# Optimization experiments

Measured on AMD Instinct MI355X. Metric: run time of the kernel, lower is better.

## Reference

```python
import jax, jax.numpy as jnp
from jax import lax
import numpy as np

Z, Y, X = 41, 256, 256  # sparse_shape = grid_size[::-1]
N_VOX = 60000
C_IN = 4
DN = ('NCDHW', 'OIDHW', 'NCDHW')


def _conv(x, w, stride=(1, 1, 1), pad=1):
    return lax.conv_general_dilated(x, w, stride, [(pad, pad)] * 3, dimension_numbers=DN)


def _tconv(x, w, stride=(2, 2, 2), pad=1, outpad=(0, 0, 0)):
    # torch ConvTranspose3d (weight [Cin,Cout,k,k,k]) == conv with lhs dilation,
    # spatially-flipped, in/out-swapped kernel, padding (k-1-p, k-1-p+output_padding)
    wt = jnp.flip(jnp.swapaxes(w, 0, 1), axis=(2, 3, 4))
    padding = [(2 - pad, 2 - pad + op) for op in outpad]  # k=3
    return lax.conv_general_dilated(x, wt, (1, 1, 1), padding, lhs_dilation=stride, dimension_numbers=DN)


def _bn_relu(y, s, b, m):
    # eval-mode BN folded into per-channel scale/shift, then ReLU, then restrict
    # to the sparse active-site mask (spconv only stores features at active sites)
    return jax.nn.relu(y * s[None, :, None, None, None] + b[None, :, None, None, None]) * m


def _forward(feats, params, coords, batch_size):
    (w1, s1, b1, w2a, s2a, b2a, w2b, s2b, b2b, w3a, s3a, b3a, w3b, s3b, b3b,
     w4a, s4a, b4a, w4b, s4b, b4b, w5a, s5a, b5a, w5b, s5b, b5b) = params
    B = batch_size
    bi, zi, yi, xi = coords[:, 0], coords[:, 1], coords[:, 2], coords[:, 3]
    dense = jnp.zeros((B, C_IN, Z, Y, X), feats.dtype).at[bi, :, zi, yi, xi].set(feats)
    m0 = jnp.zeros((B, 1, Z, Y, X), feats.dtype).at[bi, 0, zi, yi, xi].set(1.0)
    one = jnp.ones((1, 1, 3, 3, 3), feats.dtype)
    # conv1: SparseConv3d k3 s1 p1 -> active set dilates
    m1 = (_conv(m0, one) > 0).astype(feats.dtype)
    x = _bn_relu(_conv(dense, w1), s1, b1, m1)
    # conv2: SparseConv3d s2 + SubMConv3d (mask unchanged for subm)
    m2 = (_conv(m1, one, (2, 2, 2)) > 0).astype(feats.dtype)
    x = _bn_relu(_conv(x, w2a, (2, 2, 2)), s2a, b2a, m2)
    x = _bn_relu(_conv(x, w2b), s2b, b2b, m2)
    # conv3
    m3 = (_conv(m2, one, (2, 2, 2)) > 0).astype(feats.dtype)
    x = _bn_relu(_conv(x, w3a, (2, 2, 2)), s3a, b3a, m3)
    x = _bn_relu(_conv(x, w3b), s3b, b3b, m3)
    # deconv4: SparseConvTranspose3d s2 + subm
    m4 = (_tconv(m3, one) > 0).astype(feats.dtype)
    x = _bn_relu(_tconv(x, w4a), s4a, b4a, m4)
    x = _bn_relu(_conv(x, w4b), s4b, b4b, m4)
    # deconv5: output_padding (0,3,3) restores full Y/X resolution
    m5 = (_tconv(m4, one, outpad=(0, 3, 3)) > 0).astype(feats.dtype)
    x = _bn_relu(_tconv(x, w5a, outpad=(0, 3, 3)), s5a, b5a, m5)
    x = _bn_relu(_conv(x, w5b), s5b, b5b, m5)
    return x  # dense [B, 32, Z, Y, X]; zeros at inactive sites


def setup_inputs() -> dict:
    rng = np.random.default_rng(0)
    flat = rng.choice(Z * Y * X, size=N_VOX, replace=False)
    zi = (flat // (Y * X)).astype(np.int32)
    rem = flat % (Y * X)
    yi = (rem // X).astype(np.int32)
    xi = (rem % X).astype(np.int32)
    coords = np.stack([np.zeros(N_VOX, np.int32), zi, yi, xi], axis=1)

    def w(o, i):
        return jnp.asarray((rng.standard_normal((o, i, 3, 3, 3)) * 0.05).astype(np.float32))

    def scale(c):
        return jnp.asarray(rng.uniform(0.5, 1.5, c).astype(np.float32))

    def shift(c):
        return jnp.asarray((rng.standard_normal(c) * 0.1).astype(np.float32))

    return {
        'occ_voxel_features': jnp.asarray(rng.standard_normal((N_VOX, C_IN)).astype(np.float32)),
        'occ_voxel_coords': jnp.asarray(coords),
        'batch_size': 1,
        'w1': w(16, 4), 's1': scale(16), 'b1': shift(16),
        'w2a': w(32, 16), 's2a': scale(32), 'b2a': shift(32),
        'w2b': w(32, 32), 's2b': scale(32), 'b2b': shift(32),
        'w3a': w(64, 32), 's3a': scale(64), 'b3a': shift(64),
        'w3b': w(64, 64), 's3b': scale(64), 'b3b': shift(64),
        'w4a': w(64, 32), 's4a': scale(32), 'b4a': shift(32),  # transpose weight [Cin,Cout,...]
        'w4b': w(32, 32), 's4b': scale(32), 'b4b': shift(32),
        'w5a': w(32, 32), 's5a': scale(32), 'b5a': shift(32),
        'w5b': w(32, 32), 's5b': scale(32), 'b5b': shift(32),
    }


def reference(occ_voxel_features, occ_voxel_coords, batch_size,
              w1, s1, b1, w2a, s2a, b2a, w2b, s2b, b2b,
              w3a, s3a, b3a, w3b, s3b, b3b,
              w4a, s4a, b4a, w4b, s4b, b4b,
              w5a, s5a, b5a, w5b, s5b, b5b):
    params = (w1, s1, b1, w2a, s2a, b2a, w2b, s2b, b2b, w3a, s3a, b3a, w3b, s3b, b3b,
              w4a, s4a, b4a, w4b, s4b, b4b, w5a, s5a, b5a, w5b, s5b, b5b)
    return _forward(occ_voxel_features, params, occ_voxel_coords, batch_size)
```

## Files before the change

kernel.cpp:

```cpp
#include <hip/hip_runtime.h>
#include <hip/hip_bf16.h>
#include <stdint.h>

namespace {

constexpr int Z0 = 41, Y0 = 256, X0 = 256;
constexpr int Z2 = 21, Y2 = 128, X2 = 128;
constexpr int Z3 = 11, Y3 = 64,  X3 = 64;
constexpr int Z4 = 21, Y4 = 127, X4 = 127;
constexpr int NV0 = Z0 * Y0 * X0;
constexpr int NV2 = Z2 * Y2 * X2;
constexpr int NV3 = Z3 * Y3 * X3;
constexpr int NV4 = Z4 * Y4 * X4;

constexpr int ZP0 = 43, YP0 = 258, XP0 = 258; constexpr int NP0 = ZP0 * YP0 * XP0;
constexpr int ZP2 = 23, YP2 = 130, XP2 = 130; constexpr int NP2 = ZP2 * YP2 * XP2;
constexpr int ZP3 = 13, YP3 = 66,  XP3 = 66;  constexpr int NP3 = ZP3 * YP3 * XP3;
constexpr int ZP4 = 23, YP4 = 129, XP4 = 129; constexpr int NP4 = ZP4 * YP4 * XP4;

using bf16 = __hip_bfloat16;
typedef __attribute__((ext_vector_type(8))) short s16x8;
typedef __attribute__((ext_vector_type(4))) float f32x4;

__device__ inline unsigned f2b(float f) {
    return (unsigned)__builtin_bit_cast(unsigned short, __float2bfloat16(f));
}

__device__ inline int xcd_swz(int bid, int nwg) {
    int q = nwg >> 3, r = nwg & 7;
    int x = bid & 7, j = bid >> 3;
    return (x < r ? x * (q + 1) : r * (q + 1) + (x - r) * q) + j;
}

__device__ inline void glds16(const bf16* g, void* l) {
    __builtin_amdgcn_global_load_lds(
        (const __attribute__((address_space(1))) void*)g,
        (__attribute__((address_space(3))) void*)l, 16, 0, 0);
}

__global__ __launch_bounds__(256) void sentinel_k(float* out) { out[0] = 12345.0f; }

__global__ __launch_bounds__(256) void scatter_k(const float* __restrict__ feats,
                                                 const int* __restrict__ coords,
                                                 bf16* __restrict__ dense,
                                                 uint8_t* __restrict__ m0, int n) {
    int v = blockIdx.x * 256 + threadIdx.x;
    if (v >= n) return;
    int z = coords[v * 4 + 1], y = coords[v * 4 + 2], x = coords[v * 4 + 3];
    m0[(z * Y0 + y) * X0 + x] = 1;
    int pp = ((z + 1) * YP0 + (y + 1)) * XP0 + (x + 1);
    uint2 u;
    u.x = f2b(feats[v * 4 + 0]) | (f2b(feats[v * 4 + 1]) << 16);
    u.y = f2b(feats[v * 4 + 2]) | (f2b(feats[v * 4 + 3]) << 16);
    *(uint2*)(dense + (size_t)pp * 4) = u;
}

template <int C>
__global__ __launch_bounds__(256) void halo_zero_k(bf16* __restrict__ buf,
                                                   int Zi, int Yi, int Xi,
                                                   int Zp, int Yp, int Xp) {
    int i = blockIdx.x * 256 + threadIdx.x;
    int tot = Zp * Yp * Xp;
    if (i >= tot) return;
    int x = i % Xp; int t = i / Xp; int y = t % Yp; int z = t / Yp;
    bool halo = (z < 1) | (z > Zi) | (y < 1) | (y > Yi) | (x < 1) | (x > Xi);
    if (!halo) return;
    uint4 zz = make_uint4(0, 0, 0, 0);
    uint4* p = (uint4*)(buf + (size_t)i * C);
#pragma unroll
    for (int j = 0; j < C / 8; ++j) p[j] = zz;
}

__global__ __launch_bounds__(256) void repack_frag_k(const float* __restrict__ w,
                                                     bf16* __restrict__ wf,
                                                     int CIN, int COUT, int TRANS) {
    int NT = COUT / 16, KT = CIN / 32;
    int i = blockIdx.x * 256 + threadIdx.x;
    int total = 27 * NT * KT * 64;
    if (i >= total) return;
    int lane = i & 63; int t = i >> 6;
    int kt = t % KT; t /= KT; int nt = t % NT; int tap = t / NT;
    int co = nt * 16 + (lane & 15);
    int ci0 = kt * 32 + (lane >> 4) * 8;
    unsigned e[8];
#pragma unroll
    for (int j = 0; j < 8; ++j) {
        int ci = ci0 + j;
        int src = TRANS ? ((ci * COUT + co) * 27 + tap) : ((co * CIN + ci) * 27 + tap);
        e[j] = f2b(w[src]);
    }
    uint4 u;
    u.x = e[0] | (e[1] << 16); u.y = e[2] | (e[3] << 16);
    u.z = e[4] | (e[5] << 16); u.w = e[6] | (e[7] << 16);
    ((uint4*)wf)[i] = u;
}

__global__ __launch_bounds__(256) void repack_frag_c16_k(const float* __restrict__ w,
                                                         bf16* __restrict__ wf) {
    int i = blockIdx.x * 256 + threadIdx.x;
    int total = 14 * 2 * 64;
    if (i >= total) return;
    int lane = i & 63; int t = i >> 6;
    int nt = t & 1; int p = t >> 1;
    int lg = lane >> 4, lr = lane & 15;
    int co = nt * 16 + lr;
    unsigned e[8];
#pragma unroll
    for (int j = 0; j < 8; ++j) {
        int tap = 2 * p + (lg >> 1);
        int ci = (lg & 1) * 8 + j;
        e[j] = (tap < 27) ? f2b(w[(co * 16 + ci) * 27 + tap]) : 0u;
    }
    uint4 u;
    u.x = e[0] | (e[1] << 16); u.y = e[2] | (e[3] << 16);
    u.z = e[4] | (e[5] << 16); u.w = e[6] | (e[7] << 16);
    ((uint4*)wf)[i] = u;
}

__global__ __launch_bounds__(256) void repack_frag_l1_k(const float* __restrict__ w,
                                                        bf16* __restrict__ wf) {
    int i = blockIdx.x * 256 + threadIdx.x;
    if (i >= 256) return;
    int lane = i & 63, kb = i >> 6;
    int lg = lane >> 4, lr = lane & 15;
    unsigned e[8];
#pragma unroll
    for (int j = 0; j < 8; ++j) {
        int tap = kb * 8 + lg * 2 + (j >> 2);
        int ci = j & 3;
        e[j] = (tap < 27) ? f2b(w[(lr * 4 + ci) * 27 + tap]) : 0u;
    }
    uint4 u;
    u.x = e[0] | (e[1] << 16); u.y = e[2] | (e[3] << 16);
    u.z = e[4] | (e[5] << 16); u.w = e[6] | (e[7] << 16);
    ((uint4*)wf)[i] = u;
}

__global__ __launch_bounds__(256) void dilate_k(const uint8_t* __restrict__ in,
                                                uint8_t* __restrict__ out,
                                                int Zi, int Yi, int Xi,
                                                int Zo, int Yo, int Xo, int stride) {
    int idx = blockIdx.x * 256 + threadIdx.x;
    int total = Zo * Yo * Xo;
    if (idx >= total) return;
    int x = idx % Xo; int t = idx / Xo; int y = t % Yo; int z = t / Yo;
    int YX = Yi * Xi;
    uint8_t r = 0;
    for (int kz = 0; kz < 3; ++kz) {
        int zi = z * stride + kz - 1;
        if ((unsigned)zi >= (unsigned)Zi) continue;
        for (int ky = 0; ky < 3; ++ky) {
            int yi = y * stride + ky - 1;
            if ((unsigned)yi >= (unsigned)Yi) continue;
            for (int kx = 0; kx < 3; ++kx) {
                int xi = x * stride + kx - 1;
                if ((unsigned)xi >= (unsigned)Xi) continue;
                r |= in[zi * YX + yi * Xi + xi];
            }
        }
    }
    out[idx] = r ? 1 : 0;
}

__global__ __launch_bounds__(256) void dilate4_k(const uint8_t* __restrict__ in,
                                                 uint8_t* __restrict__ out,
                                                 int Z, int Y, int X) {
    int ngx = X >> 2;
    int g = blockIdx.x * 256 + threadIdx.x;
    int total = Z * Y * ngx;
    if (g >= total) return;
    int gx = g % ngx; int t = g / ngx; int y = t % Y; int z = t / Y;
    const int YX = Y * X;
    unsigned r = 0;
    for (int kz = 0; kz < 3; ++kz) {
        int zi = z + kz - 1;
        if ((unsigned)zi >= (unsigned)Z) continue;
        for (int ky = 0; ky < 3; ++ky) {
            int yi = y + ky - 1;
            if ((unsigned)yi >= (unsigned)Y) continue;
            const unsigned* rw = (const unsigned*)(in + zi * YX + yi * X);
            unsigned u1 = rw[gx];
            unsigned u0 = gx ? rw[gx - 1] : 0u;
            unsigned u2 = (gx + 1 < ngx) ? rw[gx + 1] : 0u;
            r |= u1 | ((u1 << 8) | (u0 >> 24)) | ((u1 >> 8) | (u2 << 24));
        }
    }
    r |= r >> 4; r |= r >> 2; r |= r >> 1; r &= 0x01010101u;
    ((unsigned*)out)[g] = r;
}

__global__ __launch_bounds__(256) void tdilate_k(const uint8_t* __restrict__ in,
                                                 uint8_t* __restrict__ out,
                                                 int Zi, int Yi, int Xi,
                                                 int Zo, int Yo, int Xo) {
    int idx = blockIdx.x * 256 + threadIdx.x;
    int total = Zo * Yo * Xo;
    if (idx >= total) return;
    int x = idx % Xo; int t = idx / Xo; int y = t % Yo; int z = t / Yo;
    int YX = Yi * Xi;
    uint8_t r = 0;
    for (int kz = 0; kz < 3; ++kz) {
        int tz = z + 1 - kz;
        if (tz & 1) continue;
        int zi = tz >> 1;
        if ((unsigned)zi >= (unsigned)Zi) continue;
        for (int ky = 0; ky < 3; ++ky) {
            int ty = y + 1 - ky;
            if (ty & 1) continue;
            int yi = ty >> 1;
            if ((unsigned)yi >= (unsigned)Yi) continue;
            for (int kx = 0; kx < 3; ++kx) {
                int tx = x + 1 - kx;
                if (tx & 1) continue;
                int xi = tx >> 1;
                if ((unsigned)xi >= (unsigned)Xi) continue;
                r |= in[zi * YX + yi * Xi + xi];
            }
        }
    }
    out[idx] = r ? 1 : 0;
}

__global__ __launch_bounds__(256) void tdilate4_k(const uint8_t* __restrict__ in,
                                                  uint8_t* __restrict__ out,
                                                  int Zi, int Yi, int Xi,
                                                  int Zo, int Yo, int Xo) {
    int ngx = Xo >> 2;
    int g = blockIdx.x * 256 + threadIdx.x;
    int total = Zo * Yo * ngx;
    if (g >= total) return;
    int gx = g % ngx; int t = g / ngx; int y = t % Yo; int z = t / Yo;
    int YX = Yi * Xi;
    int j0 = gx * 2;
    unsigned r0 = 0, r1 = 0, r2 = 0, r3 = 0;
    for (int kz = 0; kz < 3; ++kz) {
        int tz = z + 1 - kz;
        if (tz & 1) continue;
        int zi = tz >> 1;
        if ((unsigned)zi >= (unsigned)Zi) continue;
        for (int ky = 0; ky < 3; ++ky) {
            int ty = y + 1 - ky;
            if (ty & 1) continue;
            int yi = ty >> 1;
            if ((unsigned)yi >= (unsigned)Yi) continue;
            const uint8_t* rp = in + zi * YX + yi * Xi;
            unsigned b0 = (j0 < Xi) ? rp[j0] : 0u;
            unsigned b1 = (j0 + 1 < Xi) ? rp[j0 + 1] : 0u;
            unsigned b2 = (j0 + 2 < Xi) ? rp[j0 + 2] : 0u;
            r0 |= b0; r1 |= b0 | b1; r2 |= b1; r3 |= b1 | b2;
        }
    }
    unsigned rr = (r0 ? 1u : 0u) | (r1 ? 0x100u : 0u) | (r2 ? 0x10000u : 0u) | (r3 ? 0x1000000u : 0u);
    ((unsigned*)out)[g] = rr;
}

__global__ __launch_bounds__(256, 3) void conv_roll_k(
    const bf16* __restrict__ in, const bf16* __restrict__ wfrag,
    const float* __restrict__ scale, const float* __restrict__ shift,
    const uint8_t* __restrict__ mask, float* __restrict__ outf,
    int Zo, int Yo, int Xo, int Ypi, int Xpi, int nx) {
    constexpr int ROWB = 34 * 64;
    constexpr int SLABB = 4 * ROWB;
    __shared__ uint4 ring4[4 * SLABB / 16];
    char* ring = (char*)ring4;

    const int No = Zo * Yo * Xo;
    const int bid = xcd_swz(blockIdx.x, gridDim.x);
    const int tx = bid % nx, ty = bid / nx;
    const int y0 = ty * 2, x0 = tx * 32;

    const int tid = threadIdx.x;
    const int w = tid >> 6, lane = tid & 63;
    const int lg = lane >> 4, lr = lane & 15;
    const int yr = w >> 1, ch = w & 1;

    auto stage = [&](int zp) {
        int zs = zp <= Zo + 1 ? zp : Zo + 1;
        char* slab = ring + (zp & 3) * SLABB + w * ROWB;
        const bf16* pb = in + ((size_t)zs * Ypi + (y0 + w)) * (size_t)Xpi * 32 + (size_t)x0 * 32;
#pragma unroll
        for (int k = 0; k < 3; ++k) {
            int u = k * 64 + lane;
            if (k < 2 || lane < 8) {
                int usw = u ^ ((u >> 3) & 7);
                glds16(pb + usw * 8, slab + u * 16);
            }
        }
    };

    const uint4* gw = (const uint4*)wfrag;
    uint4 breg[27];
#pragma unroll
    for (int t = 0; t < 27; ++t) breg[t] = gw[(t * 2 + ch) * 64 + lane];

    stage(0); stage(1); stage(2);

    int asw[2][3];
#pragma unroll
    for (int xh = 0; xh < 2; ++xh)
#pragma unroll
        for (int dx = 0; dx < 3; ++dx) {
            int b = (xh * 16 + lr + dx) * 64 + lg * 16;
            asw[xh][dx] = b ^ (((b >> 7) & 7) << 4);
        }

    const int co = ch * 16 + lr;
    const float sc = scale[co], sh = shift[co];

    asm volatile("s_waitcnt vmcnt(0)" ::: "memory");
    __builtin_amdgcn_s_barrier();

    for (int z = 0; z < Zo; ++z) {
        stage(z + 3);

        f32x4 acc0 = (f32x4){0, 0, 0, 0}, acc1 = (f32x4){0, 0, 0, 0};
#pragma unroll
        for (int dz = 0; dz < 3; ++dz) {
            const char* slab = ring + ((z + dz) & 3) * SLABB;
#pragma unroll
            for (int dy = 0; dy < 3; ++dy) {
                const char* rowp = slab + (yr + dy) * ROWB;
#pragma unroll
                for (int dx = 0; dx < 3; ++dx) {
                    const int tap = dz * 9 + dy * 3 + dx;
                    uint4 a0 = *(const uint4*)(rowp + asw[0][dx]);
                    uint4 a1 = *(const uint4*)(rowp + asw[1][dx]);
                    acc0 = __builtin_amdgcn_mfma_f32_16x16x32_bf16(
                        __builtin_bit_cast(s16x8, a0), __builtin_bit_cast(s16x8, breg[tap]),
                        acc0, 0, 0, 0);
                    acc1 = __builtin_amdgcn_mfma_f32_16x16x32_bf16(
                        __builtin_bit_cast(s16x8, a1), __builtin_bit_cast(s16x8, breg[tap]),
                        acc1, 0, 0, 0);
                }
            }
        }

        const size_t rowbase = ((size_t)z * Yo + (y0 + yr)) * Xo + x0;
#pragma unroll
        for (int xh = 0; xh < 2; ++xh) {
            const size_t idx0 = rowbase + xh * 16 + lg * 4;
            uchar4 mk = *(const uchar4*)(mask + idx0);
            float mm[4] = {mk.x ? 1.f : 0.f, mk.y ? 1.f : 0.f,
                           mk.z ? 1.f : 0.f, mk.w ? 1.f : 0.f};
            f32x4 a = xh ? acc1 : acc0;
            f32x4 o;
#pragma unroll
            for (int r = 0; r < 4; ++r)
                o[r] = fmaxf(fmaf(a[r], sc, sh), 0.f) * mm[r];
            *(f32x4*)(outf + (size_t)co * No + idx0) = o;
        }

        asm volatile("s_waitcnt vmcnt(2)" ::: "memory");
        __builtin_amdgcn_s_barrier();
    }
}

template <bool FINAL>
__global__ __launch_bounds__(512, 4) void conv_lds_k(
    const bf16* __restrict__ in, const bf16* __restrict__ wfrag,
    const float* __restrict__ scale, const float* __restrict__ shift,
    const uint8_t* __restrict__ mask, bf16* __restrict__ out, float* __restrict__ outf,
    int Zo, int Yo, int Xo, int Ypi, int Xpi, int Ypo, int Xpo, int nx, int ny) {
    constexpr int ROWB = 34 * 64;
    __shared__ uint4 tile4[36 * ROWB / 16];
    char* tile = (char*)tile4;

    const int No = Zo * Yo * Xo;
    const int bid = xcd_swz(blockIdx.x, gridDim.x);
    int tx = bid % nx; int tt = bid / nx; int ty = tt % ny; int tz = tt / ny;
    const int z0 = tz * 4, y0 = ty * 4, x0 = tx * 32;

    const int tid = threadIdx.x;
    const int w = tid >> 6, lane = tid & 63, lg = lane >> 4, lr = lane & 15;

    int anywork;
    {
        int row = tid >> 5, xl = tid & 31;
        int zz = z0 + (row >> 2), yy = y0 + (row & 3), xx = x0 + xl;
        int ok = (zz < Zo) && (yy < Yo) && (xx < Xo) && mask[((size_t)zz * Yo + yy) * Xo + xx];
        anywork = __syncthreads_or(ok);
    }

    f32x4 acc[4][2];
#pragma unroll
    for (int s = 0; s < 4; ++s) { acc[s][0] = (f32x4){0,0,0,0}; acc[s][1] = (f32x4){0,0,0,0}; }

    if (anywork) {
        const int lsw = (lane ^ ((lane >> 3) & 7)) * 8;
        for (int rr = w; rr < 36; rr += 8) {
            int dz = rr / 6, dy = rr % 6;
            const bf16* g = in + ((size_t)(z0 + dz) * Ypi + (y0 + dy)) * Xpi * 32 + (size_t)x0 * 32;
            char* l = tile + rr * ROWB;
            glds16(g + lsw, l);
            glds16(g + 512 + lsw, l + 1024);
            if (lane < 8) glds16(g + 1024 + lane * 8, l + 2048);
        }
        asm volatile("s_waitcnt vmcnt(0)" ::: "memory");
        __syncthreads();

        int rbB[4], bsw[4][3];
#pragma unroll
        for (int s = 0; s < 4; ++s) {
            int lrow = 2 * w + (s >> 1);
            rbB[s] = ((lrow >> 2) * 6 + (lrow & 3)) * ROWB;
            int xpart = (s & 1) * 16 + lr;
#pragma unroll
            for (int dx = 0; dx < 3; ++dx) {
                int b = (xpart + dx) * 64 + lg * 16;
                bsw[s][dx] = b ^ (((b >> 7) & 7) << 4);
            }
        }

        const uint4* gw = (const uint4*)wfrag;
#pragma unroll 1
        for (int dz = 0; dz < 3; ++dz) {
#pragma unroll
            for (int dy = 0; dy < 3; ++dy) {
                const int rowoff = (dz * 6 + dy) * ROWB;
#pragma unroll
                for (int dx = 0; dx < 3; ++dx) {
                    const int tap = dz * 9 + dy * 3 + dx;
                    uint4 b0 = gw[(tap * 2 + 0) * 64 + lane];
                    uint4 b1 = gw[(tap * 2 + 1) * 64 + lane];
                    uint4 ua[4];
#pragma unroll
                    for (int s = 0; s < 4; ++s)
                        ua[s] = *(const uint4*)(tile + rbB[s] + rowoff + bsw[s][dx]);
#pragma unroll
                    for (int s = 0; s < 4; ++s) {
                        acc[s][0] = __builtin_amdgcn_mfma_f32_16x16x32_bf16(
                            __builtin_bit_cast(s16x8, ua[s]),
                            __builtin_bit_cast(s16x8, b0), acc[s][0], 0, 0, 0);
                        acc[s][1] = __builtin_amdgcn_mfma_f32_16x16x32_bf16(
                            __builtin_bit_cast(s16x8, ua[s]),
                            __builtin_bit_cast(s16x8, b1), acc[s][1], 0, 0, 0);
                    }
                }
            }
        }
    }

#pragma unroll
    for (int s = 0; s < 4; ++s) {
        int lrow = 2 * w + (s >> 1);
        int zz = z0 + (lrow >> 2), yy = y0 + (lrow & 3);
        int xv = x0 + (s & 1) * 16 + lg * 4;
        bool rowok = (zz < Zo) && (yy < Yo);
        if (!rowok) continue;
        size_t idx0 = ((size_t)zz * Yo + yy) * Xo + xv;
        float mm[4];
#pragma unroll
        for (int r = 0; r < 4; ++r)
            mm[r] = (xv + r < Xo && mask[idx0 + r]) ? 1.f : 0.f;
        if constexpr (FINAL) {
#pragma unroll
            for (int nt = 0; nt < 2; ++nt) {
                int co = nt * 16 + lr;
                float sc = scale[co], sh = shift[co];
                f32x4 o;
#pragma unroll
                for (int r = 0; r < 4; ++r)
                    o[r] = fmaxf(fmaf(acc[s][nt][r], sc, sh), 0.f) * mm[r];
                if (xv + 3 < Xo) {
                    *(f32x4*)(outf + (size_t)co * No + idx0) = o;
                } else {
#pragma unroll
                    for (int r = 0; r < 4; ++r)
                        if (xv + r < Xo) outf[(size_t)co * No + idx0 + r] = o[r];
                }
            }
        } else {
            int opd = ((zz + 1) * Ypo + (yy + 1)) * Xpo + (xv + 1);
#pragma unroll
            for (int nt = 0; nt < 2; ++nt) {
                int co = nt * 16 + lr;
                float sc = scale[co], sh = shift[co];
#pragma unroll
                for (int r = 0; r < 4; ++r) {
                    if (xv + r >= Xo) continue;
                    float yv = fmaxf(fmaf(acc[s][nt][r], sc, sh), 0.f) * mm[r];
                    out[(size_t)(opd + r) * 32 + co] = __float2bfloat16(yv);
                }
            }
        }
    }
}

template <int CIN, int COUT, int STRIDE, int BLK, bool FINAL>
__global__ __launch_bounds__(BLK, ((CIN <= 32 && COUT <= 32) ? 4 : 2)) void conv_mfma_k(
    const bf16* __restrict__ in, const bf16* __restrict__ wfrag,
    const float* __restrict__ scale, const float* __restrict__ shift,
    const uint8_t* __restrict__ mask, bf16* __restrict__ out, float* __restrict__ outf,
    int Zo, int Yo, int Xo, int Ypi, int Xpi, int Ypo, int Xpo) {
    constexpr int NT = COUT / 16;
    constexpr int KT = CIN / 32;
    const int No = Zo * Yo * Xo;
    const int bid = xcd_swz(blockIdx.x, gridDim.x);
    const int tid = threadIdx.x;
    const int wv = tid >> 6, lane = tid & 63;
    const int lg = lane >> 4, lr = lane & 15;
    const int v0 = bid * BLK + wv * 64;
    if (v0 >= No) return;

    int vm = v0 + lane;
    bool mw = (vm < No) && (mask[vm] != 0);
    const bool anywork = (__ballot(mw) != 0ull);

    f32x4 acc[4][NT];
#pragma unroll
    for (int s = 0; s < 4; ++s)
#pragma unroll
        for (int nt = 0; nt < NT; ++nt) acc[s][nt] = (f32x4){0.f, 0.f, 0.f, 0.f};

    const uint4* gw = (const uint4*)wfrag;

    if (anywork) {
        int pA[4];
#pragma unroll
        for (int s = 0; s < 4; ++s) {
            int vr = v0 + s * 16 + lr;
            if (vr >= No) vr = 0;
            int zz = vr / (Yo * Xo); int rr = vr - zz * (Yo * Xo);
            int yy = rr / Xo; int xx = rr - yy * Xo;
            pA[s] = (((zz * STRIDE + 1) * Ypi + (yy * STRIDE + 1)) * Xpi + (xx * STRIDE + 1)) * CIN + lg * 8;
        }
#pragma unroll
        for (int tap = 0; tap < 27; ++tap) {
            const int kz = tap / 9, r9 = tap - kz * 9, ky = r9 / 3, kx = r9 - ky * 3;
            const int toff = (((kz - 1) * Ypi + (ky - 1)) * Xpi + (kx - 1)) * CIN;
            uint4 ub[NT][KT];
#pragma unroll
            for (int nt = 0; nt < NT; ++nt)
#pragma unroll
                for (int kt = 0; kt < KT; ++kt)
                    ub[nt][kt] = gw[((tap * NT + nt) * KT + kt) * 64 + lane];
            uint4 ua[4][KT];
#pragma unroll
            for (int s = 0; s < 4; ++s)
#pragma unroll
                for (int kt = 0; kt < KT; ++kt)
                    ua[s][kt] = *(const uint4*)(in + pA[s] + toff + kt * 32);
#pragma unroll
            for (int s = 0; s < 4; ++s)
#pragma unroll
                for (int kt = 0; kt < KT; ++kt)
#pragma unroll
                    for (int nt = 0; nt < NT; ++nt)
                        acc[s][nt] = __builtin_amdgcn_mfma_f32_16x16x32_bf16(
                            __builtin_bit_cast(s16x8, ua[s][kt]),
                            __builtin_bit_cast(s16x8, ub[nt][kt]), acc[s][nt], 0, 0, 0);
        }
    }

#pragma unroll
    for (int s = 0; s < 4; ++s) {
        const int vb = v0 + s * 16 + lg * 4;
        int opd[4]; float mm[4]; bool ok[4];
#pragma unroll
        for (int r = 0; r < 4; ++r) {
            int v = vb + r;
            ok[r] = v < No;
            int vc = ok[r] ? v : 0;
            mm[r] = (ok[r] && mask[vc]) ? 1.f : 0.f;
            int zz = vc / (Yo * Xo); int rr = vc - zz * (Yo * Xo);
            int yy = rr / Xo; int xx = rr - yy * Xo;
            opd[r] = FINAL ? vc : ((zz + 1) * Ypo + (yy + 1)) * Xpo + (xx + 1);
        }
#pragma unroll
        for (int nt = 0; nt < NT; ++nt) {
            int co = nt * 16 + lr;
            float sc = scale[co], sh = shift[co];
#pragma unroll
            for (int r = 0; r < 4; ++r) {
                if (!ok[r]) continue;
                float yv = fmaxf(fmaf(acc[s][nt][r], sc, sh), 0.f) * mm[r];
                if constexpr (FINAL) outf[(size_t)co * No + opd[r]] = yv;
                else out[(size_t)opd[r] * COUT + co] = __float2bfloat16(yv);
            }
        }
    }
}

__global__ __launch_bounds__(256, 4) void conv_s2c16_k(
    const bf16* __restrict__ in, const bf16* __restrict__ wfrag,
    const float* __restrict__ scale, const float* __restrict__ shift,
    const uint8_t* __restrict__ mask, bf16* __restrict__ out,
    int Zo, int Yo, int Xo, int Ypi, int Xpi, int Ypo, int Xpo) {
    const int No = Zo * Yo * Xo;
    const int bid = xcd_swz(blockIdx.x, gridDim.x);
    const int tid = threadIdx.x;
    const int wv = tid >> 6, lane = tid & 63;
    const int lg = lane >> 4, lr = lane & 15;
    const int v0 = bid * 256 + wv * 64;
    if (v0 >= No) return;

    int vm = v0 + lane;
    bool mw = (vm < No) && (mask[vm] != 0);
    const bool anywork = (__ballot(mw) != 0ull);

    f32x4 acc[4][2];
#pragma unroll
    for (int s = 0; s < 4; ++s) { acc[s][0] = (f32x4){0,0,0,0}; acc[s][1] = (f32x4){0,0,0,0}; }

    if (anywork) {
        const uint4* gw = (const uint4*)wfrag;
        const int choff = (lg & 1) * 8;
        const int tb = lg >> 1;
        int toffl[14];
#pragma unroll
        for (int p = 0; p < 14; ++p) {
            int tp = 2 * p + tb;
            if (tp >= 27) tp = 0;
            int kz = tp / 9, r9 = tp - kz * 9, ky = r9 / 3, kx = r9 - ky * 3;
            toffl[p] = ((kz * Ypi + ky) * Xpi + kx) * 16;
        }
        int pA[4];
#pragma unroll
        for (int s = 0; s < 4; ++s) {
            int vr = v0 + s * 16 + lr;
            if (vr >= No) vr = 0;
            int zz = vr / (Yo * Xo); int rr = vr - zz * (Yo * Xo);
            int yy = rr / Xo; int xx = rr - yy * Xo;
            pA[s] = (((zz * 2) * Ypi + (yy * 2)) * Xpi + (xx * 2)) * 16 + choff;
        }
#pragma unroll
        for (int p = 0; p < 14; ++p) {
            uint4 b0 = gw[(p * 2 + 0) * 64 + lane];
            uint4 b1 = gw[(p * 2 + 1) * 64 + lane];
            uint4 ua[4];
#pragma unroll
            for (int s = 0; s < 4; ++s)
                ua[s] = *(const uint4*)(in + pA[s] + toffl[p]);
#pragma unroll
            for (int s = 0; s < 4; ++s) {
                acc[s][0] = __builtin_amdgcn_mfma_f32_16x16x32_bf16(
                    __builtin_bit_cast(s16x8, ua[s]),
                    __builtin_bit_cast(s16x8, b0), acc[s][0], 0, 0, 0);
                acc[s][1] = __builtin_amdgcn_mfma_f32_16x16x32_bf16(
                    __builtin_bit_cast(s16x8, ua[s]),
                    __builtin_bit_cast(s16x8, b1), acc[s][1], 0, 0, 0);
            }
        }
    }

#pragma unroll
    for (int s = 0; s < 4; ++s) {
        const int vb = v0 + s * 16 + lg * 4;
        int opd[4]; float mm[4]; bool ok[4];
#pragma unroll
        for (int r = 0; r < 4; ++r) {
            int v = vb + r;
            ok[r] = v < No;
            int vc = ok[r] ? v : 0;
            mm[r] = (ok[r] && mask[vc]) ? 1.f : 0.f;
            int zz = vc / (Yo * Xo); int rr = vc - zz * (Yo * Xo);
            int yy = rr / Xo; int xx = rr - yy * Xo;
            opd[r] = ((zz + 1) * Ypo + (yy + 1)) * Xpo + (xx + 1);
        }
#pragma unroll
        for (int nt = 0; nt < 2; ++nt) {
            int co = nt * 16 + lr;
            float sc = scale[co], sh = shift[co];
#pragma unroll
            for (int r = 0; r < 4; ++r) {
                if (!ok[r]) continue;
                float yv = fmaxf(fmaf(acc[s][nt][r], sc, sh), 0.f) * mm[r];
                out[(size_t)opd[r] * 32 + co] = __float2bfloat16(yv);
            }
        }
    }
}

template <int CIN, int COUT>
__global__ __launch_bounds__(256, 4) void tconv_mfma_k(
    const bf16* __restrict__ in, const bf16* __restrict__ wfrag,
    const float* __restrict__ scale, const float* __restrict__ shift,
    const uint8_t* __restrict__ mask, bf16* __restrict__ out,
    int Zo, int Yo, int Xo, int Ypi, int Xpi, int Ypo, int Xpo) {
    constexpr int NT = COUT / 16;
    constexpr int KT = CIN / 32;
    const int oct = blockIdx.y;
    const int pz = oct >> 2, py = (oct >> 1) & 1, px = oct & 1;
    const int Zq = (Zo - pz + 1) >> 1, Yq = (Yo - py + 1) >> 1, Xq = (Xo - px + 1) >> 1;
    const int Nq = Zq * Yq * Xq;
    const int YXq = Yq * Xq;
    const int bid = xcd_swz(blockIdx.x, gridDim.x);
    const int tid = threadIdx.x;
    const int wv = tid >> 6, lane = tid & 63;
    const int lg = lane >> 4, lr = lane & 15;
    const int v0 = bid * 256 + wv * 64;
    if (v0 >= Nq) return;

    bool mw = false;
    {
        int q = v0 + lane;
        if (q < Nq) {
            int zq = q / YXq; int rr = q - zq * YXq; int yq = rr / Xq; int xq = rr - yq * Xq;
            int zz = 2 * zq + pz, yy = 2 * yq + py, xx = 2 * xq + px;
            mw = mask[(zz * Yo + yy) * Xo + xx] != 0;
        }
    }
    const bool anywork = (__ballot(mw) != 0ull);

    f32x4 acc[4][NT];
#pragma unroll
    for (int s = 0; s < 4; ++s)
#pragma unroll
        for (int nt = 0; nt < NT; ++nt) acc[s][nt] = (f32x4){0.f, 0.f, 0.f, 0.f};

    const uint4* gw = (const uint4*)wfrag;

    if (anywork) {
        int pA[4];
#pragma unroll
        for (int s = 0; s < 4; ++s) {
            int q = v0 + s * 16 + lr;
            if (q >= Nq) q = 0;
            int zq = q / YXq; int rr = q - zq * YXq; int yq = rr / Xq; int xq = rr - yq * Xq;
            pA[s] = (((zq + 1) * Ypi + (yq + 1)) * Xpi + (xq + 1)) * CIN + lg * 8;
        }
        const int nkz = 1 + pz, nky = 1 + py, nkx = 1 + px;
        for (int iz = 0; iz < nkz; ++iz) {
            const int kz = pz ? (iz ? 2 : 0) : 1;
            const int dz = (pz && !iz) ? 1 : 0;
            for (int iy = 0; iy < nky; ++iy) {
                const int ky = py ? (iy ? 2 : 0) : 1;
                const int dy = (py && !iy) ? 1 : 0;
                for (int ix = 0; ix < nkx; ++ix) {
                    const int kx = px ? (ix ? 2 : 0) : 1;
                    const int dx = (px && !ix) ? 1 : 0;
                    const int tap = kz * 9 + ky * 3 + kx;
                    const int toff = ((dz * Ypi + dy) * Xpi + dx) * CIN;
                    uint4 ub[NT][KT];
#pragma unroll
                    for (int nt = 0; nt < NT; ++nt)
#pragma unroll
                        for (int kt = 0; kt < KT; ++kt)
                            ub[nt][kt] = gw[((tap * NT + nt) * KT + kt) * 64 + lane];
                    uint4 ua[4][KT];
#pragma unroll
                    for (int s = 0; s < 4; ++s)
#pragma unroll
                        for (int kt = 0; kt < KT; ++kt)
                            ua[s][kt] = *(const uint4*)(in + pA[s] + toff + kt * 32);
#pragma unroll
                    for (int s = 0; s < 4; ++s)
#pragma unroll
                        for (int kt = 0; kt < KT; ++kt)
#pragma unroll
                            for (int nt = 0; nt < NT; ++nt)
                                acc[s][nt] = __builtin_amdgcn_mfma_f32_16x16x32_bf16(
                                    __builtin_bit_cast(s16x8, ua[s][kt]),
                                    __builtin_bit_cast(s16x8, ub[nt][kt]), acc[s][nt], 0, 0, 0);
                }
            }
        }
    }

#pragma unroll
    for (int s = 0; s < 4; ++s) {
        const int vb = v0 + s * 16 + lg * 4;
        int opd[4]; float mm[4]; bool ok[4];
#pragma unroll
        for (int r = 0; r < 4; ++r) {
            int q = vb + r;
            ok[r] = q < Nq;
            int qc = ok[r] ? q : 0;
            int zq = qc / YXq; int rr = qc - zq * YXq; int yq = rr / Xq; int xq = rr - yq * Xq;
            int zz = 2 * zq + pz, yy = 2 * yq + py, xx = 2 * xq + px;
            mm[r] = (ok[r] && mask[(zz * Yo + yy) * Xo + xx]) ? 1.f : 0.f;
            opd[r] = ((zz + 1) * Ypo + (yy + 1)) * Xpo + (xx + 1);
        }
#pragma unroll
        for (int nt = 0; nt < NT; ++nt) {
            int co = nt * 16 + lr;
            float sc = scale[co], sh = shift[co];
#pragma unroll
            for (int r = 0; r < 4; ++r) {
                if (!ok[r]) continue;
                float yv = fmaxf(fmaf(acc[s][nt][r], sc, sh), 0.f) * mm[r];
                out[(size_t)opd[r] * COUT + co] = __float2bfloat16(yv);
            }
        }
    }
}

__global__ __launch_bounds__(256, 4) void conv_l1_mfma_k(
    const bf16* __restrict__ in, const bf16* __restrict__ wfrag,
    const float* __restrict__ scale, const float* __restrict__ shift,
    const uint8_t* __restrict__ mask, bf16* __restrict__ out,
    int Zo, int Yo, int Xo, int Ypi, int Xpi, int Ypo, int Xpo) {
    const int No = Zo * Yo * Xo;
    const int bid = xcd_swz(blockIdx.x, gridDim.x);
    const int tid = threadIdx.x;
    const int wv = tid >> 6, lane = tid & 63;
    const int lg = lane >> 4, lr = lane & 15;
    const int v0 = bid * 256 + wv * 64;
    if (v0 >= No) return;

    int vm = v0 + lane;
    bool mw = (vm < No) && (mask[vm] != 0);
    const bool anywork = (__ballot(mw) != 0ull);

    f32x4 acc[4];
#pragma unroll
    for (int s = 0; s < 4; ++s) acc[s] = (f32x4){0.f, 0.f, 0.f, 0.f};

    if (anywork) {
        const uint4* gw = (const uint4*)wfrag;
        uint4 bu[4];
#pragma unroll
        for (int kb = 0; kb < 4; ++kb) bu[kb] = gw[kb * 64 + lane];

        int vtf[4][2];
#pragma unroll
        for (int kb = 0; kb < 4; ++kb)
#pragma unroll
            for (int u = 0; u < 2; ++u) {
                int tp = kb * 8 + lg * 2 + u;
                int kz = tp / 9, r9 = tp - kz * 9, ky = r9 / 3, kx = r9 - ky * 3;
                vtf[kb][u] = (tp < 27) ? (((kz - 1) * Ypi + (ky - 1)) * Xpi + (kx - 1)) : 0;
            }

        int pV[4];
#pragma unroll
        for (int s = 0; s < 4; ++s) {
            int vr = v0 + s * 16 + lr;
            if (vr >= No) vr = 0;
            int zz = vr / (Yo * Xo); int rr = vr - zz * (Yo * Xo);
            int yy = rr / Xo; int xx = rr - yy * Xo;
            pV[s] = ((zz + 1) * Ypi + (yy + 1)) * Xpi + (xx + 1);
        }

#pragma unroll
        for (int kb = 0; kb < 4; ++kb) {
#pragma unroll
            for (int s = 0; s < 4; ++s) {
                uint2 a0 = *(const uint2*)(in + (size_t)(pV[s] + vtf[kb][0]) * 4);
                uint2 a1 = *(const uint2*)(in + (size_t)(pV[s] + vtf[kb][1]) * 4);
                int4 ai; ai.x = a0.x; ai.y = a0.y; ai.z = a1.x; ai.w = a1.y;
                acc[s] = __builtin_amdgcn_mfma_f32_16x16x32_bf16(
                    __builtin_bit_cast(s16x8, ai),
                    __builtin_bit_cast(s16x8, bu[kb]), acc[s], 0, 0, 0);
            }
        }
    }

#pragma unroll
    for (int s = 0; s < 4; ++s) {
        const int vb = v0 + s * 16 + lg * 4;
        int co = lr;
        float sc = scale[co], sh = shift[co];
#pragma unroll
        for (int r = 0; r < 4; ++r) {
            int v = vb + r;
            if (v >= No) continue;
            float mm = mask[v] ? 1.f : 0.f;
            int zz = v / (Yo * Xo); int rr = v - zz * (Yo * Xo);
            int yy = rr / Xo; int xx = rr - yy * Xo;
            int opd = ((zz + 1) * Ypo + (yy + 1)) * Xpo + (xx + 1);
            float yv = fmaxf(fmaf(acc[s][r], sc, sh), 0.f) * mm;
            out[(size_t)opd * 16 + co] = __float2bfloat16(yv);
        }
    }
}

inline int nblk(int n) { return (n + 255) / 256; }
inline int cdiv(int a, int b) { return (a + b - 1) / b; }

}

extern "C" void kernel_launch(void* const* d_in, const int* in_sizes, int n_in,
                              void* d_out, int out_size, void* d_ws, size_t ws_size,
                              hipStream_t stream) {
    const float* feats = (const float*)d_in[0];
    const int* coords = (const int*)d_in[1];
    const int NVOX = in_sizes[0] / 4;

    const float *w1 = (const float*)d_in[3], *s1 = (const float*)d_in[4], *b1 = (const float*)d_in[5];
    const float *w2a = (const float*)d_in[6], *s2a = (const float*)d_in[7], *b2a = (const float*)d_in[8];
    const float *w2b = (const float*)d_in[9], *s2b = (const float*)d_in[10], *b2b = (const float*)d_in[11];
    const float *w3a = (const float*)d_in[12], *s3a = (const float*)d_in[13], *b3a = (const float*)d_in[14];
    const float *w3b = (const float*)d_in[15], *s3b = (const float*)d_in[16], *b3b = (const float*)d_in[17];
    const float *w4a = (const float*)d_in[18], *s4a = (const float*)d_in[19], *b4a = (const float*)d_in[20];
    const float *w4b = (const float*)d_in[21], *s4b = (const float*)d_in[22], *b4b = (const float*)d_in[23];
    const float *w5a = (const float*)d_in[24], *s5a = (const float*)d_in[25], *b5a = (const float*)d_in[26];
    const float *w5b = (const float*)d_in[27], *s5b = (const float*)d_in[28], *b5b = (const float*)d_in[29];

    char* ws = (char*)d_ws;
    size_t off = 0;
    auto alloc = [&](size_t bytes) -> void* {
        void* p = ws + off;
        off = (off + bytes + 255) & ~(size_t)255;
        return p;
    };

    uint8_t* m0 = (uint8_t*)alloc(NV0);
    uint8_t* m1 = (uint8_t*)alloc(NV0);
    uint8_t* m2 = (uint8_t*)alloc(NV2);
    uint8_t* m3 = (uint8_t*)alloc(NV3);
    uint8_t* m4 = (uint8_t*)alloc(NV4);
    uint8_t* m5 = (uint8_t*)alloc(NV0);

    bf16* slot0 = (bf16*)alloc((size_t)NP0 * 32 * 2);
    bf16* slot1 = (bf16*)alloc((size_t)NP0 * 16 * 2);

    bf16* dense0 = slot0;
    bf16* x1     = slot1;
    bf16* x2a    = slot0;
    bf16* x2b    = slot1;
    bf16* x3a    = slot0;
    bf16* x3b    = slot1;
    bf16* x4a    = slot0;
    bf16* x4b    = slot1;
    bf16* x5a    = slot0;

    bf16* wfL1 = (bf16*)alloc(4 * 64 * 8 * 2);
    bf16* wf2a = (bf16*)alloc((size_t)14 * 2 * 64 * 16);
    bf16* wf2b = (bf16*)alloc((size_t)27 * 2 * 1 * 64 * 16);
    bf16* wf3a = (bf16*)alloc((size_t)27 * 4 * 1 * 64 * 16);
    bf16* wf3b = (bf16*)alloc((size_t)27 * 4 * 2 * 64 * 16);
    bf16* wf4a = (bf16*)alloc((size_t)27 * 2 * 2 * 64 * 16);
    bf16* wf4b = (bf16*)alloc((size_t)27 * 2 * 1 * 64 * 16);
    bf16* wf5a = (bf16*)alloc((size_t)27 * 2 * 1 * 64 * 16);
    bf16* wf5b = (bf16*)alloc((size_t)27 * 2 * 1 * 64 * 16);
    alloc(20u << 20);

    if (off > ws_size) {
        sentinel_k<<<1, 256, 0, stream>>>((float*)d_out);
        return;
    }

    hipMemsetAsync(dense0, 0, (size_t)NP0 * 4 * 2, stream);
    hipMemsetAsync(m0, 0, NV0, stream);
    repack_frag_l1_k<<<1, 256, 0, stream>>>(w1, wfL1);
    repack_frag_c16_k<<<nblk(14 * 2 * 64), 256, 0, stream>>>(w2a, wf2a);
    repack_frag_k<<<nblk(27 * 2 * 64), 256, 0, stream>>>(w2b, wf2b, 32, 32, 0);
    repack_frag_k<<<nblk(27 * 4 * 64), 256, 0, stream>>>(w3a, wf3a, 32, 64, 0);
    repack_frag_k<<<nblk(27 * 8 * 64), 256, 0, stream>>>(w3b, wf3b, 64, 64, 0);
    repack_frag_k<<<nblk(27 * 4 * 64), 256, 0, stream>>>(w4a, wf4a, 64, 32, 1);
    repack_frag_k<<<nblk(27 * 2 * 64), 256, 0, stream>>>(w4b, wf4b, 32, 32, 0);
    repack_frag_k<<<nblk(27 * 2 * 64), 256, 0, stream>>>(w5a, wf5a, 32, 32, 1);
    repack_frag_k<<<nblk(27 * 2 * 64), 256, 0, stream>>>(w5b, wf5b, 32, 32, 0);

    scatter_k<<<nblk(NVOX), 256, 0, stream>>>(feats, coords, dense0, m0, NVOX);

    dilate4_k<<<nblk(NV0 / 4), 256, 0, stream>>>(m0, m1, Z0, Y0, X0);
    halo_zero_k<16><<<nblk(NP0), 256, 0, stream>>>(x1, Z0, Y0, X0, ZP0, YP0, XP0);
    conv_l1_mfma_k<<<nblk(NV0), 256, 0, stream>>>(
        dense0, wfL1, s1, b1, m1, x1, Z0, Y0, X0, YP0, XP0, YP0, XP0);

    dilate_k<<<nblk(NV2), 256, 0, stream>>>(m1, m2, Z0, Y0, X0, Z2, Y2, X2, 2);
    halo_zero_k<32><<<nblk(NP2), 256, 0, stream>>>(x2a, Z2, Y2, X2, ZP2, YP2, XP2);
    conv_s2c16_k<<<nblk(NV2), 256, 0, stream>>>(
        x1, wf2a, s2a, b2a, m2, x2a, Z2, Y2, X2, YP0, XP0, YP2, XP2);
    halo_zero_k<32><<<nblk(NP2), 256, 0, stream>>>(x2b, Z2, Y2, X2, ZP2, YP2, XP2);
    {
        int nx = cdiv(X2, 32), ny = cdiv(Y2, 4), nz = cdiv(Z2, 4);
        conv_lds_k<false><<<nx * ny * nz, 512, 0, stream>>>(
            x2a, wf2b, s2b, b2b, m2, x2b, nullptr, Z2, Y2, X2, YP2, XP2, YP2, XP2, nx, ny);
    }

    dilate_k<<<nblk(NV3), 256, 0, stream>>>(m2, m3, Z2, Y2, X2, Z3, Y3, X3, 2);
    halo_zero_k<64><<<nblk(NP3), 256, 0, stream>>>(x3a, Z3, Y3, X3, ZP3, YP3, XP3);
    conv_mfma_k<32, 64, 2, 64, false><<<cdiv(NV3, 64), 64, 0, stream>>>(
        x2b, wf3a, s3a, b3a, m3, x3a, nullptr, Z3, Y3, X3, YP2, XP2, YP3, XP3);
    halo_zero_k<64><<<nblk(NP3), 256, 0, stream>>>(x3b, Z3, Y3, X3, ZP3, YP3, XP3);
    conv_mfma_k<64, 64, 1, 64, false><<<cdiv(NV3, 64), 64, 0, stream>>>(
        x3a, wf3b, s3b, b3b, m3, x3b, nullptr, Z3, Y3, X3, YP3, XP3, YP3, XP3);

    tdilate_k<<<nblk(NV4), 256, 0, stream>>>(m3, m4, Z3, Y3, X3, Z4, Y4, X4);
    halo_zero_k<32><<<nblk(NP4), 256, 0, stream>>>(x4a, Z4, Y4, X4, ZP4, YP4, XP4);
    {
        int maxNq = ((Z4 + 1) >> 1) * ((Y4 + 1) >> 1) * ((X4 + 1) >> 1);
        dim3 g(nblk(maxNq), 8);
        tconv_mfma_k<64, 32><<<g, 256, 0, stream>>>(
            x3b, wf4a, s4a, b4a, m4, x4a, Z4, Y4, X4, YP3, XP3, YP4, XP4);
    }
    halo_zero_k<32><<<nblk(NP2), 256, 0, stream>>>(x4b, Z4, Y4, X4, ZP2, YP2, XP2);
    {
        int nx = cdiv(X4, 32), ny = cdiv(Y4, 4), nz = cdiv(Z4, 4);
        conv_lds_k<false><<<nx * ny * nz, 512, 0, stream>>>(
            x4a, wf4b, s4b, b4b, m4, x4b, nullptr, Z4, Y4, X4, YP4, XP4, YP2, XP2, nx, ny);
    }

    tdilate4_k<<<nblk(NV0 / 4), 256, 0, stream>>>(m4, m5, Z4, Y4, X4, Z0, Y0, X0);
    halo_zero_k<32><<<nblk(NP0), 256, 0, stream>>>(x5a, Z0, Y0, X0, ZP0, YP0, XP0);
    {
        int maxNq = ((Z0 + 1) >> 1) * (Y0 >> 1) * (X0 >> 1);
        dim3 g(nblk(maxNq), 8);
        tconv_mfma_k<32, 32><<<g, 256, 0, stream>>>(
            x4b, wf5a, s5a, b5a, m5, x5a, Z0, Y0, X0, YP2, XP2, YP0, XP0);
    }
    {
        int nx = X0 / 32, ny = Y0 / 2;
        conv_roll_k<<<nx * ny, 256, 0, stream>>>(
            x5a, wf5b, s5b, b5b, m5, (float*)d_out, Z0, Y0, X0, YP0, XP0, nx);
    }
}
```

Before: 974.3 us.

## Deepen conv ring buffer, prefetch masks, add rolling-z transposed conv kernel

The final submanifold conv kernel now uses a five-slab LDS ring with four slabs staged ahead, prefetches the next z-plane's mask words into registers, and waits less strictly on outstanding loads. Occupancy drops from three to two blocks per SM to make room for the larger ring. The deconv5 transposed conv is replaced by a new tconv_roll_k kernel. It rolls along z with an LDS ring of input slabs and per-parity-octant weights kept in registers, and it prefetches masks. The aim is to hide global load latency and reuse staged input rows across z, in exchange for lower occupancy and scattered bf16 stores.

```diff
diff --git a/kernel.cpp b/kernel.cpp
--- a/kernel.cpp
+++ b/kernel.cpp
@@ -254,14 +254,14 @@
     ((unsigned*)out)[g] = rr;
 }
 
-__global__ __launch_bounds__(256, 3) void conv_roll_k(
+__global__ __launch_bounds__(256, 2) void conv_roll_k(
     const bf16* __restrict__ in, const bf16* __restrict__ wfrag,
     const float* __restrict__ scale, const float* __restrict__ shift,
     const uint8_t* __restrict__ mask, float* __restrict__ outf,
     int Zo, int Yo, int Xo, int Ypi, int Xpi, int nx) {
     constexpr int ROWB = 34 * 64;
     constexpr int SLABB = 4 * ROWB;
-    __shared__ uint4 ring4[4 * SLABB / 16];
+    __shared__ uint4 ring4[5 * SLABB / 16];
     char* ring = (char*)ring4;
 
     const int No = Zo * Yo * Xo;
@@ -274,18 +274,13 @@
     const int lg = lane >> 4, lr = lane & 15;
     const int yr = w >> 1, ch = w & 1;
 
-    auto stage = [&](int zp) {
+    auto stagefn = [&](int zp, int slot) {
         int zs = zp <= Zo + 1 ? zp : Zo + 1;
-        char* slab = ring + (zp & 3) * SLABB + w * ROWB;
+        char* slab = ring + slot * SLABB + w * ROWB;
         const bf16* pb = in + ((size_t)zs * Ypi + (y0 + w)) * (size_t)Xpi * 32 + (size_t)x0 * 32;
-#pragma unroll
-        for (int k = 0; k < 3; ++k) {
-            int u = k * 64 + lane;
-            if (k < 2 || lane < 8) {
-                int usw = u ^ ((u >> 3) & 7);
-                glds16(pb + usw * 8, slab + u * 16);
-            }
-        }
+        int u0 = lane;      glds16(pb + (u0 ^ ((u0 >> 3) & 7)) * 8, slab + u0 * 16);
+        int u1 = 64 + lane; glds16(pb + (u1 ^ ((u1 >> 3) & 7)) * 8, slab + u1 * 16);
+        if (lane < 8) { int u2 = 128 + lane; glds16(pb + u2 * 8, slab + u2 * 16); }
     };
 
     const uint4* gw = (const uint4*)wfrag;
@@ -293,38 +288,55 @@
 #pragma unroll
     for (int t = 0; t < 27; ++t) breg[t] = gw[(t * 2 + ch) * 64 + lane];
 
-    stage(0); stage(1); stage(2);
-
-    int asw[2][3];
-#pragma unroll
-    for (int xh = 0; xh < 2; ++xh)
-#pragma unroll
-        for (int dx = 0; dx < 3; ++dx) {
-            int b = (xh * 16 + lr + dx) * 64 + lg * 16;
-            asw[xh][dx] = b ^ (((b >> 7) & 7) << 4);
-        }
+    int asw0[3], asw1[3];
+#pragma unroll
+    for (int dx = 0; dx < 3; ++dx) {
+        int b0 = (lr + dx) * 64 + lg * 16;       asw0[dx] = b0 ^ (((b0 >> 7) & 7) << 4);
+        int b1 = (16 + lr + dx) * 64 + lg * 16;  asw1[dx] = b1 ^ (((b1 >> 7) & 7) << 4);
+    }
 
     const int co = ch * 16 + lr;
     const float sc = scale[co], sh = shift[co];
 
+    stagefn(0, 0); stagefn(1, 1); stagefn(2, 2); stagefn(3, 3);
+    uint mk0, mk1;
+    {
+        const uint8_t* mrow = mask + (size_t)(y0 + yr) * Xo + x0;
+        mk0 = *(const uint*)(mrow + lg * 4);
+        mk1 = *(const uint*)(mrow + 16 + lg * 4);
+    }
     asm volatile("s_waitcnt vmcnt(0)" ::: "memory");
     __builtin_amdgcn_s_barrier();
 
+    int rs0 = 0, wslot = 4;
     for (int z = 0; z < Zo; ++z) {
-        stage(z + 3);
+        uint nk0, nk1;
+        {
+            int zn = (z + 1 < Zo) ? z + 1 : Zo - 1;
+            const uint8_t* mrow = mask + ((size_t)zn * Yo + (y0 + yr)) * Xo + x0;
+            nk0 = *(const uint*)(mrow + lg * 4);
+            nk1 = *(const uint*)(mrow + 16 + lg * 4);
+        }
+        stagefn(z + 4, wslot);
+
+        int rs1 = rs0 + 1 < 5 ? rs0 + 1 : 0;
+        int rs2 = rs1 + 1 < 5 ? rs1 + 1 : 0;
+        const char* sl_0 = ring + rs0 * SLABB;
+        const char* sl_1 = ring + rs1 * SLABB;
+        const char* sl_2 = ring + rs2 * SLABB;
 
         f32x4 acc0 = (f32x4){0, 0, 0, 0}, acc1 = (f32x4){0, 0, 0, 0};
 #pragma unroll
         for (int dz = 0; dz < 3; ++dz) {
-            const char* slab = ring + ((z + dz) & 3) * SLABB;
+            const char* slab = dz == 0 ? sl_0 : (dz == 1 ? sl_1 : sl_2);
 #pragma unroll
             for (int dy = 0; dy < 3; ++dy) {
                 const char* rowp = slab + (yr + dy) * ROWB;
 #pragma unroll
                 for (int dx = 0; dx < 3; ++dx) {
                     const int tap = dz * 9 + dy * 3 + dx;
-                    uint4 a0 = *(const uint4*)(rowp + asw[0][dx]);
-                    uint4 a1 = *(const uint4*)(rowp + asw[1][dx]);
+                    uint4 a0 = *(const uint4*)(rowp + asw0[dx]);
+                    uint4 a1 = *(const uint4*)(rowp + asw1[dx]);
                     acc0 = __builtin_amdgcn_mfma_f32_16x16x32_bf16(
                         __builtin_bit_cast(s16x8, a0), __builtin_bit_cast(s16x8, breg[tap]),
                         acc0, 0, 0, 0);
@@ -336,22 +348,159 @@
         }
 
         const size_t rowbase = ((size_t)z * Yo + (y0 + yr)) * Xo + x0;
-#pragma unroll
-        for (int xh = 0; xh < 2; ++xh) {
-            const size_t idx0 = rowbase + xh * 16 + lg * 4;
-            uchar4 mk = *(const uchar4*)(mask + idx0);
-            float mm[4] = {mk.x ? 1.f : 0.f, mk.y ? 1.f : 0.f,
-                           mk.z ? 1.f : 0.f, mk.w ? 1.f : 0.f};
-            f32x4 a = xh ? acc1 : acc0;
-            f32x4 o;
-#pragma unroll
-            for (int r = 0; r < 4; ++r)
-                o[r] = fmaxf(fmaf(a[r], sc, sh), 0.f) * mm[r];
-            *(f32x4*)(outf + (size_t)co * No + idx0) = o;
-        }
-
-        asm volatile("s_waitcnt vmcnt(2)" ::: "memory");
+        {
+            f32x4 o0, o1;
+#pragma unroll
+            for (int r = 0; r < 4; ++r) {
+                float m0f = (float)((mk0 >> (8 * r)) & 1);
+                float m1f = (float)((mk1 >> (8 * r)) & 1);
+                o0[r] = fmaxf(fmaf(acc0[r], sc, sh), 0.f) * m0f;
+                o1[r] = fmaxf(fmaf(acc1[r], sc, sh), 0.f) * m1f;
+            }
+            *(f32x4*)(outf + (size_t)co * No + rowbase + lg * 4)      = o0;
+            *(f32x4*)(outf + (size_t)co * No + rowbase + 16 + lg * 4) = o1;
+        }
+
+        asm volatile("s_waitcnt vmcnt(9)" ::: "memory");
         __builtin_amdgcn_s_barrier();
+        rs0 = rs1;
+        wslot = wslot + 1 < 5 ? wslot + 1 : 0;
+        mk0 = nk0; mk1 = nk1;
+    }
+}
+
+__global__ __launch_bounds__(256, 3) void tconv_roll_k(
+    const bf16* __restrict__ in, const bf16* __restrict__ wfrag,
+    const float* __restrict__ scale, const float* __restrict__ shift,
+    const uint8_t* __restrict__ mask, bf16* __restrict__ out,
+    int Zo, int Yo, int Xo, int Zi, int Ypi, int Xpi, int Ypo, int Xpo, int nx) {
+    constexpr int ROWB = 34 * 64;
+    constexpr int SLABB = 3 * ROWB;
+    __shared__ uint4 ring4[4 * SLABB / 16];
+    char* ring = (char*)ring4;
+
+    const int oct = blockIdx.y;
+    const int pz = oct >> 2, py = (oct >> 1) & 1, px = oct & 1;
+    const int Zq = (Zo - pz + 1) >> 1;
+
+    const int bid = xcd_swz(blockIdx.x, gridDim.x);
+    const int tx = bid % nx, ty = bid / nx;
+    const int yq0 = ty * 2, xq0 = tx * 32;
+
+    const int tid = threadIdx.x;
+    const int w = tid >> 6, lane = tid & 63;
+    const int lg = lane >> 4, lr = lane & 15;
+    const int yr = w >> 1, xh = w & 1;
+
+    const int kz0 = pz ? 0 : 1, dzo0 = pz ? 1 : 0;
+    const int ky0 = py ? 0 : 1, dyo0 = py ? 1 : 0;
+    const int kx0 = px ? 0 : 1, dxo0 = px ? 1 : 0;
+
+    auto stagefn = [&](int p, int slot) {
+        if (w < 3) {
+            int zs = p < Zi ? p : Zi - 1;
+            char* slab = ring + slot * SLABB + w * ROWB;
+            const bf16* pb = in + ((size_t)(zs + 1) * Ypi + (yq0 + 1 + w)) * (size_t)Xpi * 32
+                                + (size_t)(xq0 + 1) * 32;
+            int u0 = lane;      glds16(pb + (u0 ^ ((u0 >> 3) & 7)) * 8, slab + u0 * 16);
+            int u1 = 64 + lane; glds16(pb + (u1 ^ ((u1 >> 3) & 7)) * 8, slab + u1 * 16);
+            if (lane < 8) { int u2 = 128 + lane; glds16(pb + u2 * 8, slab + u2 * 16); }
+        }
+    };
+
+    const uint4* gw = (const uint4*)wfrag;
+    uint4 breg[2][2][2][2];
+#pragma unroll
+    for (int iz = 0; iz < 2; ++iz) {
+        int kz = iz ? 2 : kz0;
+#pragma unroll
+        for (int iy = 0; iy < 2; ++iy) {
+            int ky = iy ? 2 : ky0;
+#pragma unroll
+            for (int ix = 0; ix < 2; ++ix) {
+                int kx = ix ? 2 : kx0;
+                int tap = kz * 9 + ky * 3 + kx;
+                breg[iz][iy][ix][0] = gw[(tap * 2 + 0) * 64 + lane];
+                breg[iz][iy][ix][1] = gw[(tap * 2 + 1) * 64 + lane];
+            }
+        }
+    }
+
+    int b0 = (xh * 16 + lr + dxo0) * 64 + lg * 16;
+    int b1 = (xh * 16 + lr) * 64 + lg * 16;
+    const int aswA = b0 ^ (((b0 >> 7) & 7) << 4);
+    const int aswB = b1 ^ (((b1 >> 7) & 7) << 4);
+    const int rowA = (yr + dyo0) * ROWB;
+    const int rowB = yr * ROWB;
+
+    const float sc0 = scale[lr], sh0 = shift[lr];
+    const float sc1 = scale[16 + lr], sh1 = shift[16 + lr];
+
+    const int yout = 2 * (yq0 + yr) + py;
+    const int xb = 2 * (xq0 + xh * 16 + lg * 4) + px;
+
+    stagefn(0, 0); stagefn(1, 1); stagefn(2, 2);
+    uint2 mv;
+    mv = *(const uint2*)(mask + ((size_t)pz * Yo + yout) * Xo + (xb - px));
+    asm volatile("s_waitcnt vmcnt(0)" ::: "memory");
+    __builtin_amdgcn_s_barrier();
+
+    int rs0 = 0, wslot = 3;
+    for (int zq = 0; zq < Zq; ++zq) {
+        uint2 nv;
+        {
+            int zqn = (zq + 1 < Zq) ? zq + 1 : Zq - 1;
+            nv = *(const uint2*)(mask + ((size_t)(2 * zqn + pz) * Yo + yout) * Xo + (xb - px));
+        }
+        stagefn(zq + 3, wslot);
+
+        int rs1 = rs0 + 1 < 4 ? rs0 + 1 : 0;
+        const char* sl_0 = ring + rs0 * SLABB;
+        const char* sl_1 = ring + rs1 * SLABB;
+        const char* slz0 = pz ? sl_1 : sl_0;
+        const char* slz1 = sl_0;
+
+        f32x4 acc0 = (f32x4){0, 0, 0, 0}, acc1 = (f32x4){0, 0, 0, 0};
+#pragma unroll
+        for (int iz = 0; iz < 2; ++iz) {
+            if (iz > pz) continue;
+            const char* slab = iz ? slz1 : slz0;
+#pragma unroll
+            for (int iy = 0; iy < 2; ++iy) {
+                if (iy > py) continue;
+                const char* rowp = slab + (iy ? rowB : rowA);
+#pragma unroll
+                for (int ix = 0; ix < 2; ++ix) {
+                    if (ix > px) continue;
+                    uint4 a = *(const uint4*)(rowp + (ix ? aswB : aswA));
+                    acc0 = __builtin_amdgcn_mfma_f32_16x16x32_bf16(
+                        __builtin_bit_cast(s16x8, a),
+                        __builtin_bit_cast(s16x8, breg[iz][iy][ix][0]), acc0, 0, 0, 0);
+                    acc1 = __builtin_amdgcn_mfma_f32_16x16x32_bf16(
+                        __builtin_bit_cast(s16x8, a),
+                        __builtin_bit_cast(s16x8, breg[iz][iy][ix][1]), acc1, 0, 0, 0);
+                }
+            }
+        }
+
+        const int zout = 2 * zq + pz;
+        const size_t opdbase = ((size_t)(zout + 1) * Ypo + (yout + 1)) * Xpo;
+#pragma unroll
+        for (int r = 0; r < 4; ++r) {
+            unsigned word = (r < 2) ? mv.x : mv.y;
+            float m = (float)((word >> (px * 8 + (r & 1) * 16)) & 1);
+            float v0 = fmaxf(fmaf(acc0[r], sc0, sh0), 0.f) * m;
+            float v1 = fmaxf(fmaf(acc1[r], sc1, sh1), 0.f) * m;
+            size_t opd = opdbase + (size_t)(xb + 2 * r + 1);
+            out[opd * 32 + lr]      = __float2bfloat16(v0);
+            out[opd * 32 + 16 + lr] = __float2bfloat16(v1);
+        }
+
+        asm volatile("s_waitcnt vmcnt(20)" ::: "memory");
+        __builtin_amdgcn_s_barrier();
+        rs0 = rs1;
+        wslot = wslot + 1 < 4 ? wslot + 1 : 0;
+        mv = nv;
     }
 }
 
@@ -987,10 +1136,9 @@
     tdilate4_k<<<nblk(NV0 / 4), 256, 0, stream>>>(m4, m5, Z4, Y4, X4, Z0, Y0, X0);
     halo_zero_k<32><<<nblk(NP0), 256, 0, stream>>>(x5a, Z0, Y0, X0, ZP0, YP0, XP0);
     {
-        int maxNq = ((Z0 + 1) >> 1) * (Y0 >> 1) * (X0 >> 1);
-        dim3 g(nblk(maxNq), 8);
-        tconv_mfma_k<32, 32><<<g, 256, 0, stream>>>(
-            x4b, wf5a, s5a, b5a, m5, x5a, Z0, Y0, X0, YP2, XP2, YP0, XP0);
+        dim3 g((Y0 / 2 / 2) * (X0 / 2 / 32), 8);
+        tconv_roll_k<<<g, 256, 0, stream>>>(
+            x4b, wf5a, s5a, b5a, m5, x5a, Z0, Y0, X0, Z4, YP2, XP2, YP0, XP0, X0 / 2 / 32);
     }
     {
         int nx = X0 / 32, ny = Y0 / 2;
```

After: 866.1 us. 1.12x faster.
